# Performance work log

Hardware: AMD Instinct MI355X
Metric: run time of the kernel (lower is better)

The kernel has to match this reference:

```python
import jax, jax.numpy as jnp
import numpy as np

V, D, H, NL, C, CD, B, L = 50257, 512, 8, 4, 10, 64, 16, 512
DH = D // H
EPS = 1e-5


def layer_norm(x, g, b):
    m = jnp.mean(x, axis=-1, keepdims=True)
    v = jnp.var(x, axis=-1, keepdims=True)
    return (x - m) * jax.lax.rsqrt(v + EPS) * g + b


def setup_inputs() -> dict:
    key = jax.random.key(0)
    ks = jax.random.split(key, 16)
    s = lambda k, shape: (jax.random.normal(k, shape, jnp.float32) * 0.02)
    x = jax.random.randint(ks[0], (B, L), 0, V, dtype=jnp.int32)
    return {
        "x": x,
        "embed": s(ks[1], (V, D)),
        "pos": jax.random.normal(ks[2], (1, L, D), jnp.float32),  # nn.Parameter randn
        "Wqkv": s(ks[3], (NL, 3 * D, D)), "bqkv": jnp.zeros((NL, 3 * D)),
        "Wo": s(ks[4], (NL, D, D)), "bo": jnp.zeros((NL, D)),
        "ln1_g": jnp.ones((NL, D)), "ln1_b": jnp.zeros((NL, D)),
        "W1": s(ks[5], (NL, 4 * D, D)), "b1": jnp.zeros((NL, 4 * D)),
        "W2": s(ks[6], (NL, D, 4 * D)), "b2": jnp.zeros((NL, D)),
        "ln2_g": jnp.ones((NL, D)), "ln2_b": jnp.zeros((NL, D)),
        "cnt_ln_g": jnp.ones((V,)), "cnt_ln_b": jnp.zeros((V,)),
        "Wc": s(ks[7], (CD, V)), "bc": jnp.zeros((CD,)),
        "Wh": s(ks[8], (C, D + CD)), "bh": jnp.zeros((C,)),
    }


def _encoder(x, embed, pos, Wqkv, bqkv, Wo, bo, ln1_g, ln1_b, W1, b1, W2, b2, ln2_g, ln2_b):
    h = embed[x] + pos[:, : x.shape[1]]  # (B,L,D)
    scale = 1.0 / jnp.sqrt(jnp.float32(DH))
    for i in range(NL):
        # post-LN TransformerEncoderLayer, gelu (exact), dropout=0 (eval)
        qkv = h @ Wqkv[i].T + bqkv[i]
        q, k, v = jnp.split(qkv, 3, axis=-1)
        q = q.reshape(B, L, H, DH)
        k = k.reshape(B, L, H, DH)
        v = v.reshape(B, L, H, DH)
        att = jax.nn.softmax(jnp.einsum("bqhd,bkhd->bhqk", q, k) * scale, axis=-1)
        o = jnp.einsum("bhqk,bkhd->bqhd", att, v).reshape(B, L, D)
        h = layer_norm(h + o @ Wo[i].T + bo[i], ln1_g[i], ln1_b[i])
        ff = jax.nn.gelu(h @ W1[i].T + b1[i], approximate=False) @ W2[i].T + b2[i]
        h = layer_norm(h + ff, ln2_g[i], ln2_b[i])
    return h


def reference(x, embed, pos, Wqkv, bqkv, Wo, bo, ln1_g, ln1_b, W1, b1, W2, b2,
              ln2_g, ln2_b, cnt_ln_g, cnt_ln_b, Wc, bc, Wh, bh):
    enc = _encoder(x, embed, pos, Wqkv, bqkv, Wo, bo, ln1_g, ln1_b, W1, b1, W2, b2, ln2_g, ln2_b)
    ctx_vec = enc.mean(axis=1)  # (B,D)
    # histogram of tokens per sequence, pad (id 0) excluded: same math as
    # one_hot(x).masked_fill(x==pad).sum(1) but O(B*L) scatter-add.
    mask = (x != 0).astype(jnp.float32)
    counts = jnp.zeros((B, V), jnp.float32).at[jnp.arange(B)[:, None], x].add(mask)
    cf = jax.nn.relu(layer_norm(counts, cnt_ln_g, cnt_ln_b) @ Wc.T + bc)  # (B,CD)
    feat = jnp.concatenate([ctx_vec, cf], axis=-1)
    return feat @ Wh.T + bh  # (B,C)
```

## Files before the change

kernel.cpp:

```cpp
#include <hip/hip_runtime.h>
#include <hip/hip_bf16.h>
#include <math.h>

#define V_  50257
#define D_  512
#define H_  8
#define NL_ 4
#define C_  10
#define CD_ 64
#define B_  16
#define L_  512
#define DH_ 64

typedef __attribute__((ext_vector_type(8))) short bf16x8;
typedef __attribute__((ext_vector_type(4))) float f32x4;

__device__ inline float bf2f(unsigned short u) {
    union { unsigned int i; float f; } c; c.i = ((unsigned int)u) << 16; return c.f;
}
__device__ inline unsigned short f2bf(float f) {
    unsigned int x = __float_as_uint(f);
    unsigned int r = (x + 0x7fffu + ((x >> 16) & 1u)) >> 16;
    return (unsigned short)r;
}
__device__ inline unsigned long long pack4(float a, float b, float c, float d) {
    return (unsigned long long)f2bf(a)         |
           ((unsigned long long)f2bf(b) << 16) |
           ((unsigned long long)f2bf(c) << 32) |
           ((unsigned long long)f2bf(d) << 48);
}

__device__ inline void gload16(const unsigned short* g, unsigned short* l) {
    __builtin_amdgcn_global_load_lds(
        (const __attribute__((address_space(1))) unsigned int*)g,
        (__attribute__((address_space(3))) unsigned int*)l,
        16, 0, 0);
}

template<int BM, int BN, int WGM, int WGN, int EPI>
__global__ __launch_bounds__(256) void gemm_bf16(
    const unsigned short* __restrict__ A, int lda, long aHi, long aLo,
    const unsigned short* __restrict__ B, int ldb, long bHi, long bLo,
    void* __restrict__ Cout, int ldc, long cHi, long cLo,
    const float* __restrict__ bias,
    const unsigned short* __restrict__ resb, int ldr,
    int K, unsigned short* __restrict__ vtout)
{
    constexpr int BK = 64;
    constexpr int FM = BM / (WGM * 16);
    constexpr int FN = BN / (WGN * 16);
    constexpr int CHA = BM / 8;
    constexpr int CHB = BN / 8;
    extern __shared__ unsigned short glds[];
    unsigned short* As = glds;
    unsigned short* Bs = glds + 2 * BM * BK;

    const int z  = blockIdx.z;
    const int zh = z >> 3, zl = z & 7;
    A += zh * aHi + zl * aLo;
    B += zh * bHi + zl * bLo;
    const long coff = zh * cHi + zl * cLo;

    const int tid  = threadIdx.x;
    const int lane = tid & 63;
    const int w    = tid >> 6;
    const int wr   = w / WGN, wc = w % WGN;
    const long rowA0 = (long)blockIdx.x * BM;
    const long rowB0 = (long)blockIdx.y * BN;

    f32x4 acc[FM][FN];
    #pragma unroll
    for (int m = 0; m < FM; m++)
        #pragma unroll
        for (int n = 0; n < FN; n++)
            #pragma unroll
            for (int r = 0; r < 4; r++) acc[m][n][r] = 0.f;

    const int lr   = lane & 15;
    const int crow = lane >> 3;
    const int ccol = ((lane & 7) ^ crow) * 8;

    auto stage = [&](int bf, int k0) {
        #pragma unroll
        for (int c0 = 0; c0 < CHA / 4; c0++) {
            const int c = c0 * 4 + w;
            gload16(&A[(rowA0 + c * 8 + crow) * (long)lda + k0 + ccol],
                    &As[bf * BM * BK + c * 512]);
        }
        #pragma unroll
        for (int c0 = 0; c0 < CHB / 4; c0++) {
            const int c = c0 * 4 + w;
            gload16(&B[(rowB0 + c * 8 + crow) * (long)ldb + k0 + ccol],
                    &Bs[bf * BN * BK + c * 512]);
        }
    };

    stage(0, 0);
    int cur = 0;
    for (int k0 = 0; k0 < K; k0 += BK) {
        __syncthreads();
        if (k0 + BK < K) stage(cur ^ 1, k0 + BK);

        #pragma unroll
        for (int kh = 0; kh < 2; kh++) {
            bf16x8 af[FM], bfr[FN];
            const int sl = ((kh * 4 + (lane >> 4)) ^ (lr & 7)) * 8;
            #pragma unroll
            for (int m = 0; m < FM; m++)
                af[m] = *(const bf16x8*)
                    &As[cur * BM * BK + (wr * FM * 16 + m * 16 + lr) * BK + sl];
            #pragma unroll
            for (int n = 0; n < FN; n++)
                bfr[n] = *(const bf16x8*)
                    &Bs[cur * BN * BK + (wc * FN * 16 + n * 16 + lr) * BK + sl];
            #pragma unroll
            for (int m = 0; m < FM; m++)
                #pragma unroll
                for (int n = 0; n < FN; n++)
                    acc[m][n] = __builtin_amdgcn_mfma_f32_16x16x32_bf16(
                        af[m], bfr[n], acc[m][n], 0, 0, 0);
        }
        cur ^= 1;
    }

    const int rg = (lane >> 4) * 4;
    if constexpr (EPI == 4) {
        if (rowB0 >= 2 * D_) {
            unsigned short* T = glds;
            __syncthreads();
            #pragma unroll
            for (int m = 0; m < FM; m++)
                #pragma unroll
                for (int n = 0; n < FN; n++) {
                    const int lcol = wc * FN * 16 + n * 16 + lr;
                    const float bv = bias[(int)rowB0 + lcol];
                    #pragma unroll
                    for (int r = 0; r < 4; r++) {
                        const int lrow = wr * FM * 16 + m * 16 + rg + r;
                        T[lrow * 132 + lcol] = f2bf(acc[m][n][r] + bv);
                    }
                }
            __syncthreads();
            const int bb = (int)(rowA0 >> 9);
            const int l0 = (int)(rowA0 & 511);
            const int vcBase = (int)(rowB0 - 2 * D_);
            for (int c = tid; c < 2048; c += 256) {
                const int vc    = c & 127;
                const int ch    = c >> 7;
                const int lt2   = ch >> 3;
                const int gslot = ch & 7;
                const int gvc = vcBase + vc;
                const int hd = gvc >> 6, d = gvc & 63;
                bf16x8 o;
                #pragma unroll
                for (int j = 0; j < 8; j++)
                    o[j] = (short)T[(lt2 * 64 + gslot * 8 + j) * 132 + vc];
                *(bf16x8*)&vtout[(long)(bb * 8 + hd) * (DH_ * L_)
                                 + (long)d * 512 + l0 + lt2 * 64
                                 + ((gslot ^ (d & 7)) * 8)] = o;
            }
            return;
        }
        #pragma unroll
        for (int m = 0; m < FM; m++)
            #pragma unroll
            for (int n = 0; n < FN; n++) {
                const int col = (int)rowB0 + wc * FN * 16 + n * 16 + lr;
                const float bv = bias[col];
                #pragma unroll
                for (int r = 0; r < 4; r++) {
                    const long row = rowA0 + wr * FM * 16 + m * 16 + rg + r;
                    ((unsigned short*)Cout)[row * ldc + col] =
                        f2bf(acc[m][n][r] + bv);
                }
            }
        return;
    }

    #pragma unroll
    for (int m = 0; m < FM; m++) {
        #pragma unroll
        for (int n = 0; n < FN; n++) {
            const int col = (int)rowB0 + wc * FN * 16 + n * 16 + lr;
            const float bv = bias ? bias[col] : 0.f;
            #pragma unroll
            for (int r = 0; r < 4; r++) {
                const long row = rowA0 + wr * FM * 16 + m * 16 + rg + r;
                float v = acc[m][n][r] + bv;
                const long o = coff + row * ldc + col;
                if constexpr (EPI == 0) {
                    ((unsigned short*)Cout)[o] = f2bf(v);
                } else if constexpr (EPI == 3) {
                    ((unsigned short*)Cout)[o] =
                        f2bf(v + bf2f(resb[row * ldr + col]));
                } else {
                    float g = 0.5f * v * (1.f + erff(v * 0.70710678118f));
                    ((unsigned short*)Cout)[o] = f2bf(g);
                }
            }
        }
    }
}

__global__ __launch_bounds__(256) void attn_kernel(
    const unsigned short* __restrict__ qkv,
    const unsigned short* __restrict__ vt,
    unsigned short* __restrict__ attno)
{
    extern __shared__ unsigned short lds[];
    unsigned short* Qs = lds;
    unsigned short* Ks = lds + 4096;
    unsigned short* Ps = lds + 4096;
    unsigned short* Vb = lds + 20480;

    const int bid = blockIdx.x;
    const int z   = bid & 127;
    const int qb  = bid >> 7;
    const int b = z >> 3, hh = z & 7;
    const unsigned short* Q  = qkv + (long)b * (L_ * 3 * D_) + hh * DH_;
    const unsigned short* Kp = Q + D_;
    const int row0 = qb * 64;

    const int tid = threadIdx.x, lane = tid & 63, w = tid >> 6;
    const int lr = lane & 15, lg = lane >> 4;

    const int srow = lane >> 3;
    const int scol = ((lane & 7) ^ (srow & 7)) * 8;
    #pragma unroll
    for (int c = 0; c < 2; c++)
        gload16(&Q[(long)(row0 + (w * 2 + c) * 8 + srow) * (3 * D_) + scol],
                &Qs[(w * 2 + c) * 512]);
    #pragma unroll
    for (int c = 0; c < 16; c++)
        gload16(&Kp[(long)((c * 4 + w) * 8 + srow) * (3 * D_) + scol],
                &Ks[(c * 4 + w) * 512]);
    __syncthreads();

    f32x4 acc[32];
    #pragma unroll
    for (int n = 0; n < 32; n++)
        #pragma unroll
        for (int r = 0; r < 4; r++) acc[n][r] = 0.f;

    __builtin_amdgcn_s_setprio(1);
    #pragma unroll
    for (int ks = 0; ks < 2; ks++) {
        const int sl = ((ks * 4 + lg) ^ (lr & 7)) * 8;
        bf16x8 qf = *(const bf16x8*)&Qs[(w * 16 + lr) * 64 + sl];
        #pragma unroll
        for (int n = 0; n < 32; n++) {
            bf16x8 kf = *(const bf16x8*)&Ks[(n * 16 + lr) * 64 + sl];
            acc[n] = __builtin_amdgcn_mfma_f32_16x16x32_bf16(kf, qf, acc[n], 0, 0, 0);
        }
    }
    __builtin_amdgcn_s_setprio(0);

    constexpr float scale = 0.125f;
    float red[32];
    #pragma unroll
    for (int n = 0; n < 32; n++)
        red[n] = fmaxf(fmaxf(acc[n][0], acc[n][1]), fmaxf(acc[n][2], acc[n][3]));
    #pragma unroll
    for (int st = 16; st; st >>= 1)
        #pragma unroll
        for (int i = 0; i < 16; i++)
            if (i < st) red[i] = fmaxf(red[i], red[i + st]);
    float mx = red[0];
    mx = fmaxf(mx, __shfl_xor(mx, 16));
    mx = fmaxf(mx, __shfl_xor(mx, 32));
    const float ms = mx * scale;
    #pragma unroll
    for (int n = 0; n < 32; n++) {
        float e0 = __expf(acc[n][0] * scale - ms);
        float e1 = __expf(acc[n][1] * scale - ms);
        float e2 = __expf(acc[n][2] * scale - ms);
        float e3 = __expf(acc[n][3] * scale - ms);
        acc[n][0] = e0; acc[n][1] = e1; acc[n][2] = e2; acc[n][3] = e3;
        red[n] = (e0 + e1) + (e2 + e3);
    }
    #pragma unroll
    for (int st = 16; st; st >>= 1)
        #pragma unroll
        for (int i = 0; i < 16; i++)
            if (i < st) red[i] += red[i + st];
    float s = red[0];
    s += __shfl_xor(s, 16);
    s += __shfl_xor(s, 32);
    const float rinv = 1.f / s;

    __syncthreads();

    const long vbase = (long)z * (DH_ * L_);
    const int vrow2 = lane >> 5;
    const int vs    = lane & 31;
    const int q     = w * 16 + lr;
    f32x4 accO[4];
    #pragma unroll
    for (int dt = 0; dt < 4; dt++)
        #pragma unroll
        for (int r = 0; r < 4; r++) accO[dt][r] = 0.f;

    #pragma unroll
    for (int hf = 0; hf < 2; hf++) {
        if (hf) __syncthreads();
        #pragma unroll
        for (int c = 0; c < 8; c++) {
            const int ch = c * 4 + w;
            const int dloc = ch * 2 + vrow2;
            gload16(&vt[vbase + (long)dloc * 512 + hf * 256 + vs * 8],
                    &Vb[ch * 512]);
        }
        #pragma unroll
        for (int n = 0; n < 16; n++) {
            const int slot = (n * 2 + (lg >> 1)) ^ (lr & 7);
            unsigned long long pk = pack4(acc[hf * 16 + n][0], acc[hf * 16 + n][1],
                                          acc[hf * 16 + n][2], acc[hf * 16 + n][3]);
            *(unsigned long long*)&Ps[q * 256 + slot * 8 + (lg & 1) * 4] = pk;
        }
        __syncthreads();
        __builtin_amdgcn_s_setprio(1);
        #pragma unroll
        for (int kstep = 0; kstep < 8; kstep++) {
            const int sl = ((kstep * 4 + lg) ^ (lr & 7)) * 8;
            bf16x8 pf = *(const bf16x8*)&Ps[q * 256 + sl];
            #pragma unroll
            for (int dt = 0; dt < 4; dt++) {
                bf16x8 vf = *(const bf16x8*)&Vb[(dt * 16 + lr) * 256 + sl];
                accO[dt] = __builtin_amdgcn_mfma_f32_16x16x32_bf16(vf, pf, accO[dt], 0, 0, 0);
            }
        }
        __builtin_amdgcn_s_setprio(0);
    }

    unsigned short* op = attno + (long)(b * L_ + row0 + q) * D_ + hh * DH_;
    #pragma unroll
    for (int dt = 0; dt < 4; dt++) {
        unsigned long long pk = pack4(accO[dt][0] * rinv, accO[dt][1] * rinv,
                                      accO[dt][2] * rinv, accO[dt][3] * rinv);
        *(unsigned long long*)&op[dt * 16 + lg * 4] = pk;
    }
}

__global__ __launch_bounds__(256) void cvtall_kernel(
    const float* __restrict__ s0, const float* __restrict__ s1,
    const float* __restrict__ s2, const float* __restrict__ s3,
    unsigned short* __restrict__ dst)
{
    const long n0 = 786432, n1 = 262144, n2 = 1048576;
    long i4 = (long)blockIdx.x * 256 + threadIdx.x;
    const float* s; long off;
    if (i4 < n0)                { s = s0; off = 0; }
    else if (i4 < n0 + n1)      { s = s1; off = n0; }
    else if (i4 < n0 + n1 + n2) { s = s2; off = n0 + n1; }
    else                        { s = s3; off = n0 + n1 + n2; }
    float4 v = ((const float4*)s)[i4 - off];
    *(unsigned long long*)&dst[i4 * 4] = pack4(v.x, v.y, v.z, v.w);
}

__global__ __launch_bounds__(256) void embed_kernel(
    const int* __restrict__ x, const float* __restrict__ emb,
    const float* __restrict__ pos, unsigned short* __restrict__ hb)
{
    const long row = blockIdx.x;
    const int tok = x[row];
    const int l = (int)(row & (L_ - 1));
    const int d0 = threadIdx.x * 2;
    float2 e = *(const float2*)&emb[(long)tok * D_ + d0];
    float2 p = *(const float2*)&pos[(long)l * D_ + d0];
    float a0 = e.x + p.x, a1 = e.y + p.y;
    unsigned int pk = (unsigned int)f2bf(a0) | ((unsigned int)f2bf(a1) << 16);
    *(unsigned int*)&hb[row * D_ + d0] = pk;
}

__global__ __launch_bounds__(256) void ln_kernel(
    const unsigned short* __restrict__ t, const float* __restrict__ g,
    const float* __restrict__ bb, unsigned short* __restrict__ hb)
{
    const int lane = threadIdx.x & 63;
    const long row = (long)blockIdx.x * 4 + (threadIdx.x >> 6);
    const unsigned short* x = t + row * D_;
    float v[8];
    bf16x8 d = *(const bf16x8*)&x[lane * 8];
    #pragma unroll
    for (int j = 0; j < 8; j++) v[j] = bf2f((unsigned short)d[j]);
    float s = 0.f;
    #pragma unroll
    for (int j = 0; j < 8; j++) s += v[j];
    #pragma unroll
    for (int o = 32; o; o >>= 1) s += __shfl_xor(s, o);
    const float m = s * (1.f / D_);
    float q = 0.f;
    #pragma unroll
    for (int j = 0; j < 8; j++) { float dd = v[j] - m; q += dd * dd; }
    #pragma unroll
    for (int o = 32; o; o >>= 1) q += __shfl_xor(q, o);
    const float rr = rsqrtf(q * (1.f / D_) + 1e-5f);
    bf16x8 ob;
    #pragma unroll
    for (int j = 0; j < 8; j++) {
        int dd = lane * 8 + j;
        ob[j] = (short)f2bf((v[j] - m) * rr * g[dd] + bb[dd]);
    }
    *(bf16x8*)&hb[row * D_ + lane * 8] = ob;
}

__global__ __launch_bounds__(512) void ctxmean_kernel(
    const unsigned short* __restrict__ hb, float* __restrict__ ctx)
{
    const int b = blockIdx.x, seg = blockIdx.y;
    const int d = threadIdx.x;
    float s = 0.f;
    #pragma unroll 4
    for (int l = seg * 64; l < seg * 64 + 64; l++)
        s += bf2f(hb[((long)b * L_ + l) * D_ + d]);
    atomicAdd(&ctx[b * D_ + d], s * (1.f / L_));
}

__global__ __launch_bounds__(256) void zero_kernel(float* __restrict__ p, long n)
{
    long i = (long)blockIdx.x * 256 + threadIdx.x;
    if (i < n) p[i] = 0.f;
}

__global__ __launch_bounds__(256) void hist_kernel(
    const int* __restrict__ x, float* __restrict__ counts)
{
    const int i = blockIdx.x * 256 + threadIdx.x;
    if (i >= B_ * L_) return;
    const int tok = x[i];
    if (tok != 0) atomicAdd(&counts[(long)(i >> 9) * V_ + tok], 1.0f);
}

__global__ __launch_bounds__(256) void cstats_kernel(
    const float* __restrict__ counts, float* __restrict__ statsraw)
{
    const int b = blockIdx.x, seg = blockIdx.y;
    const int n0 = seg * 3142;
    const int n1 = min(n0 + 3142, V_);
    float s1 = 0.f, s2 = 0.f;
    for (int v = n0 + threadIdx.x; v < n1; v += 256) {
        float c = counts[(long)b * V_ + v];
        s1 += c; s2 += c * c;
    }
    #pragma unroll
    for (int o = 32; o; o >>= 1) { s1 += __shfl_xor(s1, o); s2 += __shfl_xor(s2, o); }
    __shared__ float r1[4], r2[4];
    if ((threadIdx.x & 63) == 0) { r1[threadIdx.x >> 6] = s1; r2[threadIdx.x >> 6] = s2; }
    __syncthreads();
    if (threadIdx.x == 0) {
        atomicAdd(&statsraw[b * 2],     r1[0] + r1[1] + r1[2] + r1[3]);
        atomicAdd(&statsraw[b * 2 + 1], r2[0] + r2[1] + r2[2] + r2[3]);
    }
}

__global__ __launch_bounds__(256) void wct_kernel(
    const float* __restrict__ Wc, const float* __restrict__ g,
    float* __restrict__ WcT)
{
    __shared__ float tile[64][65];
    __shared__ float gs[64];
    const int v0 = blockIdx.x * 64;
    const int t = threadIdx.x;
    if (t < 64) gs[t] = (v0 + t < V_) ? g[v0 + t] : 0.f;
    const int vv = t & 63;
    const int vg = v0 + vv;
    #pragma unroll
    for (int r = 0; r < 16; r++) {
        int cd = r * 4 + (t >> 6);
        tile[cd][vv] = (vg < V_) ? Wc[(long)cd * V_ + vg] : 0.f;
    }
    __syncthreads();
    #pragma unroll
    for (int r = 0; r < 16; r++) {
        int v2 = r * 4 + (t >> 6);
        int cd = t & 63;
        if (v0 + v2 < V_)
            WcT[(long)(v0 + v2) * 64 + cd] = tile[cd][v2] * gs[v2];
    }
}

__global__ __launch_bounds__(256) void sgbred_kernel(
    const float* __restrict__ Wc, const float* __restrict__ g,
    const float* __restrict__ bb, float* __restrict__ sgb)
{
    const int cd = blockIdx.x >> 2, chunk = blockIdx.x & 3;
    const int n0 = chunk * 12565;
    const int n1 = min(n0 + 12565, V_);
    float s1 = 0.f, s2 = 0.f;
    for (int v = n0 + threadIdx.x; v < n1; v += 256) {
        float wv = Wc[(long)cd * V_ + v];
        s1 += wv * g[v];
        s2 += wv * bb[v];
    }
    #pragma unroll
    for (int o = 32; o; o >>= 1) { s1 += __shfl_xor(s1, o); s2 += __shfl_xor(s2, o); }
    __shared__ float r1[4], r2[4];
    if ((threadIdx.x & 63) == 0) { r1[threadIdx.x >> 6] = s1; r2[threadIdx.x >> 6] = s2; }
    __syncthreads();
    if (threadIdx.x == 0) {
        atomicAdd(&sgb[cd * 2],     r1[0] + r1[1] + r1[2] + r1[3]);
        atomicAdd(&sgb[cd * 2 + 1], r2[0] + r2[1] + r2[2] + r2[3]);
    }
}

__global__ __launch_bounds__(256) void cgather_kernel(
    const int* __restrict__ x, const float* __restrict__ WcT,
    float* __restrict__ dot)
{
    const int b = blockIdx.x, seg = blockIdx.y;
    const int wv = threadIdx.x >> 6, lane = threadIdx.x & 63;
    float s = 0.f;
    #pragma unroll
    for (int i = 0; i < 16; i++) {
        int tok = x[b * L_ + seg * 64 + wv * 16 + i];
        if (tok != 0) s += WcT[(long)tok * 64 + lane];
    }
    atomicAdd(&dot[b * 64 + lane], s);
}

__global__ void cfinal_kernel(
    const float* __restrict__ dot, const float* __restrict__ statsraw,
    const float* __restrict__ sgb, const float* __restrict__ bc,
    float* __restrict__ cf)
{
    const int b = blockIdx.x, cd = threadIdx.x;
    const float s1 = statsraw[b * 2], s2 = statsraw[b * 2 + 1];
    const float m = s1 * (1.f / V_);
    const float r = rsqrtf(s2 * (1.f / V_) - m * m + 1e-5f);
    float v = r * (dot[b * 64 + cd] - m * sgb[cd * 2]) + sgb[cd * 2 + 1] + bc[cd];
    cf[b * CD_ + cd] = fmaxf(v, 0.f);
}

__global__ __launch_bounds__(256) void final_kernel(
    const float* __restrict__ ctx, const float* __restrict__ cf,
    const float* __restrict__ Wh, const float* __restrict__ bh,
    float* __restrict__ out)
{
    const int p = threadIdx.x;
    if (p >= B_ * C_) return;
    const int b = p / C_, c = p % C_;
    float s = bh[c];
    const float* wrow = Wh + (long)c * (D_ + CD_);
    for (int d = 0; d < D_; d++) s += ctx[b * D_ + d] * wrow[d];
    for (int j = 0; j < CD_; j++) s += cf[b * CD_ + j] * wrow[D_ + j];
    out[p] = s;
}

extern "C" void kernel_launch(void* const* d_in, const int* in_sizes, int n_in,
                              void* d_out, int out_size, void* d_ws, size_t ws_size,
                              hipStream_t stream)
{
    const int*   x      = (const int*)  d_in[0];
    const float* embedw = (const float*)d_in[1];
    const float* pos    = (const float*)d_in[2];
    const float* Wqkv   = (const float*)d_in[3];
    const float* bqkv   = (const float*)d_in[4];
    const float* Wo     = (const float*)d_in[5];
    const float* bo     = (const float*)d_in[6];
    const float* ln1g   = (const float*)d_in[7];
    const float* ln1b   = (const float*)d_in[8];
    const float* W1     = (const float*)d_in[9];
    const float* b1     = (const float*)d_in[10];
    const float* W2     = (const float*)d_in[11];
    const float* b2     = (const float*)d_in[12];
    const float* ln2g   = (const float*)d_in[13];
    const float* ln2b   = (const float*)d_in[14];
    const float* cgv    = (const float*)d_in[15];
    const float* cbv    = (const float*)d_in[16];
    const float* Wc     = (const float*)d_in[17];
    const float* bc     = (const float*)d_in[18];
    const float* Wh     = (const float*)d_in[19];
    const float* bh     = (const float*)d_in[20];
    float* out = (float*)d_out;

    char* ws = (char*)d_ws;
    size_t off = 0;
    auto alloc = [&](size_t bytes) -> void* {
        void* p = ws + off;
        off += (bytes + 255) & ~(size_t)255;
        return p;
    };
    unsigned short* hb    = (unsigned short*)alloc((size_t)B_ * L_ * D_ * 2);
    unsigned short* qkv   = (unsigned short*)alloc((size_t)B_ * L_ * 3 * D_ * 2);
    unsigned short* vt    = (unsigned short*)alloc((size_t)B_ * H_ * DH_ * L_ * 2);
    unsigned short* ff1   = (unsigned short*)alloc((size_t)B_ * L_ * 4 * D_ * 2);
    unsigned short* attno = (unsigned short*)alloc((size_t)B_ * L_ * D_ * 2);
    unsigned short* tbuf  = (unsigned short*)alloc((size_t)B_ * L_ * D_ * 2);
    unsigned short* wqb   = (unsigned short*)alloc((size_t)NL_ * 3 * D_ * D_ * 2);
    unsigned short* wob   = (unsigned short*)alloc((size_t)NL_ * D_ * D_ * 2);
    unsigned short* w1b   = (unsigned short*)alloc((size_t)NL_ * 4 * D_ * D_ * 2);
    unsigned short* w2b   = (unsigned short*)alloc((size_t)NL_ * 4 * D_ * D_ * 2);
    float*          counts= (float*)alloc((size_t)B_ * V_ * 4);
    float*          statsraw = (float*)alloc(B_ * 2 * 4);
    float*          sgb   = (float*)alloc(CD_ * 2 * 4);
    float*          dot   = (float*)alloc(B_ * CD_ * 4);
    float*          ctx   = (float*)alloc(B_ * D_ * 4);
    float*          cf    = (float*)alloc(B_ * CD_ * 4);
    float*          WcT   = (float*)qkv;

    cvtall_kernel<<<12288, 256, 0, stream>>>(Wqkv, Wo, W1, W2, wqb);

    embed_kernel<<<B_*L_, 256, 0, stream>>>(x, embedw, pos, hb);

    const int lds_128 = (128 + 128) * 64 * 4;
    const int lds_64  = (64 + 128) * 64 * 4;

    for (int i = 0; i < NL_; i++) {
        gemm_bf16<128,128,2,2,4><<<dim3(64,12,1),256,lds_128,stream>>>(
            hb, 512, 0, 0,
            wqb + (size_t)i*786432, 512, 0, 0,
            qkv, 1536, 0, 0,
            bqkv + i*1536, nullptr, 0, 512, vt);
        attn_kernel<<<1024, 256, 73728, stream>>>(qkv, vt, attno);
        gemm_bf16<64,128,1,4,3><<<dim3(128,4,1),256,lds_64,stream>>>(
            attno, 512, 0, 0,
            wob + (size_t)i*262144, 512, 0, 0,
            tbuf, 512, 0, 0,
            bo + i*512, hb, 512, 512, nullptr);
        ln_kernel<<<2048,256,0,stream>>>(tbuf, ln1g + i*512, ln1b + i*512, hb);
        gemm_bf16<128,128,2,2,2><<<dim3(64,16,1),256,lds_128,stream>>>(
            hb, 512, 0, 0,
            w1b + (size_t)i*1048576, 512, 0, 0,
            ff1, 2048, 0, 0,
            b1 + i*2048, nullptr, 0, 512, nullptr);
        gemm_bf16<64,128,1,4,3><<<dim3(128,4,1),256,lds_64,stream>>>(
            ff1, 2048, 0, 0,
            w2b + (size_t)i*1048576, 2048, 0, 0,
            tbuf, 512, 0, 0,
            b2 + i*512, hb, 512, 2048, nullptr);
        ln_kernel<<<2048,256,0,stream>>>(tbuf, ln2g + i*512, ln2b + i*512, hb);
    }

    {
        long span = (((char*)cf + B_*CD_*4) - (char*)counts) / 4;
        zero_kernel<<<(span + 255)/256, 256, 0, stream>>>(counts, span);
    }
    ctxmean_kernel<<<dim3(B_,8),512,0,stream>>>(hb, ctx);
    hist_kernel<<<(B_*L_ + 255)/256, 256, 0, stream>>>(x, counts);
    cstats_kernel<<<dim3(B_,16),256,0,stream>>>(counts, statsraw);
    wct_kernel<<<(V_ + 63)/64, 256, 0, stream>>>(Wc, cgv, WcT);
    sgbred_kernel<<<256,256,0,stream>>>(Wc, cgv, cbv, sgb);
    cgather_kernel<<<dim3(B_,8),256,0,stream>>>(x, WcT, dot);
    cfinal_kernel<<<B_,64,0,stream>>>(dot, statsraw, sgb, bc, cf);
    final_kernel<<<1,256,0,stream>>>(ctx, cf, Wh, bh, out);
}
```

Baseline: 673.7 us.

## Repartition attention waves over keys and make histogram stats sparse over tokens

The attention kernel now splits the 512 keys across the four waves, with each wave covering all 64 query rows, instead of giving each wave 16 queries. Row max and row sum are combined across waves through LDS with extra barriers, and the PV product is split by head-dimension tile per wave. Separately, the dense zeroing and full-vocabulary scan of the counts buffer are replaced by zeroing only the touched entries and computing sum and sum-of-squares from the token list, since each token contributes its count once per occurrence. This relies on counts entries outside the touched set already being zero from earlier calls, and on the memory layout of statsraw through cf for the smaller zero span.

```diff
diff --git a/kernel.cpp b/kernel.cpp
--- a/kernel.cpp
+++ b/kernel.cpp
@@ -212,6 +212,8 @@
     unsigned short* Ks = lds + 4096;
     unsigned short* Ps = lds + 4096;
     unsigned short* Vb = lds + 20480;
+    float* redM = (float*)lds;
+    float* redS = (float*)lds + 256;
 
     const int bid = blockIdx.x;
     const int z   = bid & 127;
@@ -236,69 +238,101 @@
                 &Ks[(c * 4 + w) * 512]);
     __syncthreads();
 
-    f32x4 acc[32];
-    #pragma unroll
-    for (int n = 0; n < 32; n++)
-        #pragma unroll
-        for (int r = 0; r < 4; r++) acc[n][r] = 0.f;
+    f32x4 acc[4][8];
+    #pragma unroll
+    for (int qf = 0; qf < 4; qf++)
+        #pragma unroll
+        for (int n = 0; n < 8; n++)
+            #pragma unroll
+            for (int r = 0; r < 4; r++) acc[qf][n][r] = 0.f;
 
     __builtin_amdgcn_s_setprio(1);
     #pragma unroll
     for (int ks = 0; ks < 2; ks++) {
         const int sl = ((ks * 4 + lg) ^ (lr & 7)) * 8;
-        bf16x8 qf = *(const bf16x8*)&Qs[(w * 16 + lr) * 64 + sl];
-        #pragma unroll
-        for (int n = 0; n < 32; n++) {
-            bf16x8 kf = *(const bf16x8*)&Ks[(n * 16 + lr) * 64 + sl];
-            acc[n] = __builtin_amdgcn_mfma_f32_16x16x32_bf16(kf, qf, acc[n], 0, 0, 0);
+        bf16x8 qfv[4];
+        #pragma unroll
+        for (int qf = 0; qf < 4; qf++)
+            qfv[qf] = *(const bf16x8*)&Qs[(qf * 16 + lr) * 64 + sl];
+        #pragma unroll
+        for (int n = 0; n < 8; n++) {
+            bf16x8 kf = *(const bf16x8*)&Ks[(w * 128 + n * 16 + lr) * 64 + sl];
+            #pragma unroll
+            for (int qf = 0; qf < 4; qf++)
+                acc[qf][n] = __builtin_amdgcn_mfma_f32_16x16x32_bf16(
+                    kf, qfv[qf], acc[qf][n], 0, 0, 0);
         }
     }
     __builtin_amdgcn_s_setprio(0);
 
     constexpr float scale = 0.125f;
-    float red[32];
-    #pragma unroll
-    for (int n = 0; n < 32; n++)
-        red[n] = fmaxf(fmaxf(acc[n][0], acc[n][1]), fmaxf(acc[n][2], acc[n][3]));
-    #pragma unroll
-    for (int st = 16; st; st >>= 1)
-        #pragma unroll
-        for (int i = 0; i < 16; i++)
-            if (i < st) red[i] = fmaxf(red[i], red[i + st]);
-    float mx = red[0];
-    mx = fmaxf(mx, __shfl_xor(mx, 16));
-    mx = fmaxf(mx, __shfl_xor(mx, 32));
-    const float ms = mx * scale;
-    #pragma unroll
-    for (int n = 0; n < 32; n++) {
-        float e0 = __expf(acc[n][0] * scale - ms);
-        float e1 = __expf(acc[n][1] * scale - ms);
-        float e2 = __expf(acc[n][2] * scale - ms);
-        float e3 = __expf(acc[n][3] * scale - ms);
-        acc[n][0] = e0; acc[n][1] = e1; acc[n][2] = e2; acc[n][3] = e3;
-        red[n] = (e0 + e1) + (e2 + e3);
-    }
-    #pragma unroll
-    for (int st = 16; st; st >>= 1)
-        #pragma unroll
-        for (int i = 0; i < 16; i++)
-            if (i < st) red[i] += red[i + st];
-    float s = red[0];
-    s += __shfl_xor(s, 16);
-    s += __shfl_xor(s, 32);
-    const float rinv = 1.f / s;
-
+    float rmax[4];
+    #pragma unroll
+    for (int qf = 0; qf < 4; qf++) {
+        float t = -3e38f;
+        #pragma unroll
+        for (int n = 0; n < 8; n++)
+            t = fmaxf(t, fmaxf(fmaxf(acc[qf][n][0], acc[qf][n][1]),
+                               fmaxf(acc[qf][n][2], acc[qf][n][3])));
+        t = fmaxf(t, __shfl_xor(t, 16));
+        t = fmaxf(t, __shfl_xor(t, 32));
+        rmax[qf] = t;
+    }
     __syncthreads();
+    if (lg == 0) {
+        #pragma unroll
+        for (int qf = 0; qf < 4; qf++)
+            redM[w * 64 + qf * 16 + lr] = rmax[qf];
+    }
+    __syncthreads();
+    float gms[4];
+    #pragma unroll
+    for (int qf = 0; qf < 4; qf++) {
+        const int q = qf * 16 + lr;
+        gms[qf] = fmaxf(fmaxf(redM[q], redM[64 + q]),
+                        fmaxf(redM[128 + q], redM[192 + q])) * scale;
+    }
+    float rsum[4];
+    #pragma unroll
+    for (int qf = 0; qf < 4; qf++) {
+        float s = 0.f;
+        #pragma unroll
+        for (int n = 0; n < 8; n++) {
+            float e0 = __expf(acc[qf][n][0] * scale - gms[qf]);
+            float e1 = __expf(acc[qf][n][1] * scale - gms[qf]);
+            float e2 = __expf(acc[qf][n][2] * scale - gms[qf]);
+            float e3 = __expf(acc[qf][n][3] * scale - gms[qf]);
+            acc[qf][n][0] = e0; acc[qf][n][1] = e1;
+            acc[qf][n][2] = e2; acc[qf][n][3] = e3;
+            s += (e0 + e1) + (e2 + e3);
+        }
+        s += __shfl_xor(s, 16);
+        s += __shfl_xor(s, 32);
+        rsum[qf] = s;
+    }
+    if (lg == 0) {
+        #pragma unroll
+        for (int qf = 0; qf < 4; qf++)
+            redS[w * 64 + qf * 16 + lr] = rsum[qf];
+    }
+    __syncthreads();
+    float rinv[4];
+    #pragma unroll
+    for (int qf = 0; qf < 4; qf++) {
+        const int q = qf * 16 + lr;
+        rinv[qf] = 1.f / (redS[q] + redS[64 + q] + redS[128 + q] + redS[192 + q]);
+    }
 
     const long vbase = (long)z * (DH_ * L_);
     const int vrow2 = lane >> 5;
     const int vs    = lane & 31;
-    const int q     = w * 16 + lr;
+    const int myhalf = w >> 1;
+    const int rawbase = (w & 1) * 16;
     f32x4 accO[4];
     #pragma unroll
-    for (int dt = 0; dt < 4; dt++)
-        #pragma unroll
-        for (int r = 0; r < 4; r++) accO[dt][r] = 0.f;
+    for (int qt = 0; qt < 4; qt++)
+        #pragma unroll
+        for (int r = 0; r < 4; r++) accO[qt][r] = 0.f;
 
     #pragma unroll
     for (int hf = 0; hf < 2; hf++) {
@@ -310,34 +344,42 @@
             gload16(&vt[vbase + (long)dloc * 512 + hf * 256 + vs * 8],
                     &Vb[ch * 512]);
         }
-        #pragma unroll
-        for (int n = 0; n < 16; n++) {
-            const int slot = (n * 2 + (lg >> 1)) ^ (lr & 7);
-            unsigned long long pk = pack4(acc[hf * 16 + n][0], acc[hf * 16 + n][1],
-                                          acc[hf * 16 + n][2], acc[hf * 16 + n][3]);
-            *(unsigned long long*)&Ps[q * 256 + slot * 8 + (lg & 1) * 4] = pk;
+        if (myhalf == hf) {
+            #pragma unroll
+            for (int qf = 0; qf < 4; qf++) {
+                const int q = qf * 16 + lr;
+                #pragma unroll
+                for (int n = 0; n < 8; n++) {
+                    const int slot = (rawbase + n * 2 + (lg >> 1)) ^ (lr & 7);
+                    unsigned long long pk = pack4(
+                        acc[qf][n][0], acc[qf][n][1],
+                        acc[qf][n][2], acc[qf][n][3]);
+                    *(unsigned long long*)&Ps[q * 256 + slot * 8 + (lg & 1) * 4] = pk;
+                }
+            }
         }
         __syncthreads();
         __builtin_amdgcn_s_setprio(1);
         #pragma unroll
         for (int kstep = 0; kstep < 8; kstep++) {
             const int sl = ((kstep * 4 + lg) ^ (lr & 7)) * 8;
-            bf16x8 pf = *(const bf16x8*)&Ps[q * 256 + sl];
-            #pragma unroll
-            for (int dt = 0; dt < 4; dt++) {
-                bf16x8 vf = *(const bf16x8*)&Vb[(dt * 16 + lr) * 256 + sl];
-                accO[dt] = __builtin_amdgcn_mfma_f32_16x16x32_bf16(vf, pf, accO[dt], 0, 0, 0);
+            bf16x8 vf = *(const bf16x8*)&Vb[(w * 16 + lr) * 256 + sl];
+            #pragma unroll
+            for (int qt = 0; qt < 4; qt++) {
+                bf16x8 pf = *(const bf16x8*)&Ps[(qt * 16 + lr) * 256 + sl];
+                accO[qt] = __builtin_amdgcn_mfma_f32_16x16x32_bf16(
+                    vf, pf, accO[qt], 0, 0, 0);
             }
         }
         __builtin_amdgcn_s_setprio(0);
     }
 
-    unsigned short* op = attno + (long)(b * L_ + row0 + q) * D_ + hh * DH_;
-    #pragma unroll
-    for (int dt = 0; dt < 4; dt++) {
-        unsigned long long pk = pack4(accO[dt][0] * rinv, accO[dt][1] * rinv,
-                                      accO[dt][2] * rinv, accO[dt][3] * rinv);
-        *(unsigned long long*)&op[dt * 16 + lg * 4] = pk;
+    unsigned short* op = attno + (long)(b * L_ + row0) * D_ + hh * DH_;
+    #pragma unroll
+    for (int qt = 0; qt < 4; qt++) {
+        unsigned long long pk = pack4(accO[qt][0] * rinv[qt], accO[qt][1] * rinv[qt],
+                                      accO[qt][2] * rinv[qt], accO[qt][3] * rinv[qt]);
+        *(unsigned long long*)&op[(long)(qt * 16 + lr) * D_ + w * 16 + lg * 4] = pk;
     }
 }
 
@@ -422,6 +464,15 @@
     if (i < n) p[i] = 0.f;
 }
 
+__global__ __launch_bounds__(256) void zscat_kernel(
+    const int* __restrict__ x, float* __restrict__ counts)
+{
+    const int i = blockIdx.x * 256 + threadIdx.x;
+    if (i >= B_ * L_) return;
+    const int tok = x[i];
+    if (tok != 0) counts[(long)(i >> 9) * V_ + tok] = 0.f;
+}
+
 __global__ __launch_bounds__(256) void hist_kernel(
     const int* __restrict__ x, float* __restrict__ counts)
 {
@@ -431,25 +482,25 @@
     if (tok != 0) atomicAdd(&counts[(long)(i >> 9) * V_ + tok], 1.0f);
 }
 
-__global__ __launch_bounds__(256) void cstats_kernel(
-    const float* __restrict__ counts, float* __restrict__ statsraw)
-{
-    const int b = blockIdx.x, seg = blockIdx.y;
-    const int n0 = seg * 3142;
-    const int n1 = min(n0 + 3142, V_);
+__global__ __launch_bounds__(512) void cstats_kernel(
+    const int* __restrict__ x, const float* __restrict__ counts,
+    float* __restrict__ statsraw)
+{
+    const int b = blockIdx.x, t = threadIdx.x;
+    const int tok = x[b * L_ + t];
     float s1 = 0.f, s2 = 0.f;
-    for (int v = n0 + threadIdx.x; v < n1; v += 256) {
-        float c = counts[(long)b * V_ + v];
-        s1 += c; s2 += c * c;
-    }
+    if (tok != 0) { s1 = 1.f; s2 = counts[(long)b * V_ + tok]; }
     #pragma unroll
     for (int o = 32; o; o >>= 1) { s1 += __shfl_xor(s1, o); s2 += __shfl_xor(s2, o); }
-    __shared__ float r1[4], r2[4];
-    if ((threadIdx.x & 63) == 0) { r1[threadIdx.x >> 6] = s1; r2[threadIdx.x >> 6] = s2; }
+    __shared__ float r1[8], r2[8];
+    if ((t & 63) == 0) { r1[t >> 6] = s1; r2[t >> 6] = s2; }
     __syncthreads();
-    if (threadIdx.x == 0) {
-        atomicAdd(&statsraw[b * 2],     r1[0] + r1[1] + r1[2] + r1[3]);
-        atomicAdd(&statsraw[b * 2 + 1], r2[0] + r2[1] + r2[2] + r2[3]);
+    if (t == 0) {
+        float t1 = 0.f, t2 = 0.f;
+        #pragma unroll
+        for (int i = 0; i < 8; i++) { t1 += r1[i]; t2 += r2[i]; }
+        statsraw[b * 2] = t1;
+        statsraw[b * 2 + 1] = t2;
     }
 }
 
@@ -632,12 +683,13 @@
     }
 
     {
-        long span = (((char*)cf + B_*CD_*4) - (char*)counts) / 4;
-        zero_kernel<<<(span + 255)/256, 256, 0, stream>>>(counts, span);
-    }
+        long span = (((char*)cf + ((B_*CD_*4 + 255) & ~255)) - (char*)statsraw) / 4;
+        zero_kernel<<<(span + 255)/256, 256, 0, stream>>>(statsraw, span);
+    }
+    zscat_kernel<<<(B_*L_ + 255)/256, 256, 0, stream>>>(x, counts);
     ctxmean_kernel<<<dim3(B_,8),512,0,stream>>>(hb, ctx);
     hist_kernel<<<(B_*L_ + 255)/256, 256, 0, stream>>>(x, counts);
-    cstats_kernel<<<dim3(B_,16),256,0,stream>>>(counts, statsraw);
+    cstats_kernel<<<B_,512,0,stream>>>(x, counts, statsraw);
     wct_kernel<<<(V_ + 63)/64, 256, 0, stream>>>(Wc, cgv, WcT);
     sgbred_kernel<<<256,256,0,stream>>>(Wc, cgv, cbv, sgb);
     cgather_kernel<<<dim3(B_,8),256,0,stream>>>(x, WcT, dot);
```

Measured after the change: 695.6 us. 1.03x slower.
